# Performance work log

Hardware: AMD Instinct MI355X
Metric: run time of the kernel (lower is better)

The kernel has to match this reference:

```python
import jax, jax.numpy as jnp
import numpy as np

EMBED_DIM = 1024
N_HEADS = 16
HEAD_DIM = EMBED_DIM // N_HEADS


def setup_inputs() -> dict:
    key = jax.random.key(0)
    ks = jax.random.split(key, 8)
    B, Tq, Tk, C = 2, 2048, 2048, EMBED_DIM
    s = 1.0 / np.sqrt(C)
    return {
        "query": jax.random.normal(ks[0], (B, Tq, C), jnp.float32),
        "context": jax.random.normal(ks[1], (B, Tk, C), jnp.float32),
        "Wq": jax.random.normal(ks[2], (C, C), jnp.float32) * s,
        "bq": jnp.zeros((C,), jnp.float32),
        "Wkv": jax.random.normal(ks[3], (C, 2 * C), jnp.float32) * s,
        "bkv": jnp.zeros((2 * C,), jnp.float32),
        "Wo": jax.random.normal(ks[4], (C, C), jnp.float32) * s,
        "bo": jnp.zeros((C,), jnp.float32),
    }


def reference(query, context, Wq, bq, Wkv, bkv, Wo, bo):
    B, Tq, C = query.shape
    Tk = context.shape[1]
    H, D = N_HEADS, HEAD_DIM
    # projections
    q = (query @ Wq + bq).reshape(B, Tq, H, D)        # [B,Tq,H,D]
    kv = (context @ Wkv + bkv).reshape(B, Tk, 2, H, D)
    k = kv[:, :, 0]                                   # [B,Tk,H,D]
    v = kv[:, :, 1]
    scale = D ** -0.5
    # attention scores [B,H,Tq,Tk]
    attn = jnp.einsum("bqhd,bkhd->bhqk", q, k) * scale
    attn = jax.nn.softmax(attn, axis=-1)
    # dropout p=0.0 -> identity in eval / p=0
    out = jnp.einsum("bhqk,bkhd->bqhd", attn, v).reshape(B, Tq, C)
    return out @ Wo + bo
```

## Files before the change

kernel.cpp:

```cpp
#include <hip/hip_runtime.h>
#include <math.h>

typedef unsigned short u16;
typedef unsigned int u32;
typedef __attribute__((ext_vector_type(8))) short short8;
typedef __attribute__((ext_vector_type(4))) short short4v;
typedef __attribute__((ext_vector_type(4))) float f32x4;

__device__ __forceinline__ u16 f2bf(float f) {
  union { float f; unsigned u; } x; x.f = f;
  unsigned r = x.u + 0x7FFFu + ((x.u >> 16) & 1u);
  return (u16)(r >> 16);
}

__device__ __forceinline__ u32 asu(float f) {
  union { float f; u32 u; } x; x.f = f; return x.u;
}

__device__ __forceinline__ u32 pack2bf(float a, float b) {
  return __builtin_amdgcn_perm(asu(b) + 0x8000u, asu(a) + 0x8000u, 0x07060302u);
}

__device__ __forceinline__ void gld_lds16(const void* g, void* l) {
  __builtin_amdgcn_global_load_lds(
      (const __attribute__((address_space(1))) unsigned int*)g,
      (__attribute__((address_space(3))) unsigned int*)l, 16, 0, 0);
}

__global__ void pre_kernel(const float* __restrict__ q, const float* __restrict__ c,
                           const float* __restrict__ Wq, const float* __restrict__ Wkv,
                           const float* __restrict__ Wo,
                           u16* __restrict__ xq, u16* __restrict__ xc,
                           u16* __restrict__ WqT, u16* __restrict__ WkvT,
                           u16* __restrict__ WoT) {
  __shared__ float tile[32][33];
  int bx = blockIdx.x, t = threadIdx.x;
  if (bx < 8192) {
    int i = bx * 256 + t;
    const float* src = q; u16* dst = xq;
    if (i >= 1048576) { i -= 1048576; src = c; dst = xc; }
    float4 v = ((const float4*)src)[i];
    ((uint2*)dst)[i] = make_uint2(
        (unsigned)f2bf(v.x) | ((unsigned)f2bf(v.y) << 16),
        (unsigned)f2bf(v.z) | ((unsigned)f2bf(v.w) << 16));
  } else {
    int g = bx - 8192;
    int gx = g & 127, gy = g >> 7;
    const float* src; u16* dst; int N, n0;
    if (gx < 32)      { src = Wq;  dst = WqT;  N = 1024; n0 = gx * 32; }
    else if (gx < 96) { src = Wkv; dst = WkvT; N = 2048; n0 = (gx - 32) * 32; }
    else              { src = Wo;  dst = WoT;  N = 1024; n0 = (gx - 96) * 32; }
    int k0 = gy * 32;
    int tx = t & 31, ty = t >> 5;
#pragma unroll
    for (int i = 0; i < 4; ++i)
      tile[ty * 4 + i][tx] = src[(size_t)(k0 + ty * 4 + i) * N + n0 + tx];
    __syncthreads();
#pragma unroll
    for (int i = 0; i < 4; ++i)
      dst[(size_t)(n0 + ty * 4 + i) * 1024 + k0 + tx] = f2bf(tile[tx][ty * 4 + i]);
  }
}

__global__ __launch_bounds__(256) void qkv_gemm(
    const u16* __restrict__ Xq, const u16* __restrict__ Xc,
    const u16* __restrict__ WqT, const u16* __restrict__ WkvT,
    const float* __restrict__ bq, const float* __restrict__ bkv,
    u16* __restrict__ qb, u16* __restrict__ kf, u16* __restrict__ vf,
    float qscale) {
  __shared__ __align__(16) u16 smem[16896];
  u16* As = smem;
  u16* Bs = smem + 8192;
  const int tid = threadIdx.x, lane = tid & 63, wave = tid >> 6;
  const int quad = lane >> 4, cl = lane & 15;
  const int wr = (wave >> 1) * 64, wc = (wave & 1) * 64;

  int x = blockIdx.x;
  const u16 *A, *Bt; const float* bias; int N, m0, n0; bool isq;
  if (x < 256) {
    isq = true;  A = Xq; Bt = WqT;  bias = bq;  N = 1024;
    m0 = (x >> 3) * 128; n0 = (x & 7) * 128;
  } else {
    isq = false; x -= 256; A = Xc; Bt = WkvT; bias = bkv; N = 2048;
    m0 = (x >> 4) * 128; n0 = (x & 15) * 128;
  }

  f32x4 acc[4][4] = {};

  for (int k0 = 0; k0 < 1024; k0 += 64) {
#pragma unroll
    for (int it = 0; it < 4; ++it) {
      int chunk = (it * 4 + wave) * 64 + lane;
      int row = chunk >> 3, kc = (chunk & 7) * 8;
      gld_lds16(A + (size_t)(m0 + row) * 1024 + k0 + kc, As + (size_t)(it * 4 + wave) * 512);
      gld_lds16(Bt + (size_t)(n0 + row) * 1024 + k0 + kc, Bs + (size_t)(it * 4 + wave) * 512);
    }
    __syncthreads();
#pragma unroll
    for (int ks = 0; ks < 2; ++ks) {
      short8 af[4], bf[4];
#pragma unroll
      for (int mi = 0; mi < 4; ++mi)
        af[mi] = *(const short8*)(As + (wr + mi * 16 + cl) * 64 + ks * 32 + quad * 8);
#pragma unroll
      for (int ni = 0; ni < 4; ++ni)
        bf[ni] = *(const short8*)(Bs + (wc + ni * 16 + cl) * 64 + ks * 32 + quad * 8);
#pragma unroll
      for (int mi = 0; mi < 4; ++mi)
#pragma unroll
        for (int ni = 0; ni < 4; ++ni)
          acc[mi][ni] = __builtin_amdgcn_mfma_f32_16x16x32_bf16(af[mi], bf[ni], acc[mi][ni], 0, 0, 0);
    }
    __syncthreads();
  }

  if (isq) {
#pragma unroll
    for (int mi = 0; mi < 4; ++mi)
#pragma unroll
      for (int ni = 0; ni < 4; ++ni)
#pragma unroll
        for (int r = 0; r < 4; ++r) {
          int row = m0 + wr + mi * 16 + quad * 4 + r;
          int col = n0 + wc + ni * 16 + cl;
          qb[(size_t)row * 1024 + col] = f2bf((acc[mi][ni][r] + bias[col]) * qscale);
        }
    return;
  }

  const int b = m0 >> 11, kt0 = (m0 & 2047) >> 6;
  const bool kreg = (n0 < 1024);
  if (kreg) {
#pragma unroll
    for (int mi = 0; mi < 4; ++mi)
#pragma unroll
      for (int ni = 0; ni < 4; ++ni)
#pragma unroll
        for (int r = 0; r < 4; ++r)
          smem[(wr + mi * 16 + quad * 4 + r) * 132 + wc + ni * 16 + cl] =
              f2bf(acc[mi][ni][r] + bias[n0 + wc + ni * 16 + cl]);
    __syncthreads();
#pragma unroll
    for (int i = 0; i < 8; ++i) {
      int c = i * 4 + wave;
      int hs = c >> 4, ts = (c >> 3) & 1, ks = (c >> 2) & 1, idx = c & 3;
      int h = (n0 >> 6) + hs;
      size_t bhkt = ((size_t)((b * 16 + h) * 32 + kt0 + ts)) * 4096;
      short8 v = *(const short8*)(smem + (ts * 64 + idx * 16 + cl) * 132 +
                                  hs * 64 + ks * 32 + quad * 8);
      *(short8*)(kf + bhkt + (size_t)(ks * 4 + idx) * 512 + lane * 8) = v;
    }
  } else {
#pragma unroll
    for (int mi = 0; mi < 4; ++mi)
#pragma unroll
      for (int ni = 0; ni < 4; ++ni) {
        float v0 = acc[mi][ni][0] + bias[n0 + wc + ni * 16 + cl];
        float v1 = acc[mi][ni][1] + bias[n0 + wc + ni * 16 + cl];
        float v2 = acc[mi][ni][2] + bias[n0 + wc + ni * 16 + cl];
        float v3 = acc[mi][ni][3] + bias[n0 + wc + ni * 16 + cl];
        *(uint2*)(smem + (wc + ni * 16 + cl) * 132 + wr + mi * 16 + quad * 4) =
            make_uint2(pack2bf(v0, v1), pack2bf(v2, v3));
      }
    __syncthreads();
#pragma unroll
    for (int i = 0; i < 8; ++i) {
      int c = i * 4 + wave;
      int hs = c >> 4, ts = (c >> 3) & 1, ks = (c >> 2) & 1, idx = c & 3;
      int h = ((n0 - 1024) >> 6) + hs;
      size_t bhkt = ((size_t)((b * 16 + h) * 32 + kt0 + ts)) * 4096;
      const u16* src = smem + (hs * 64 + idx * 16 + cl) * 132 + ts * 64 + ks * 32 + quad * 4;
      short8 v;
      *(short4v*)&v       = *(const short4v*)(src);
      *((short4v*)&v + 1) = *(const short4v*)(src + 16);
      *(short8*)(vf + bhkt + (size_t)(ks * 4 + idx) * 512 + lane * 8) = v;
    }
  }
}

__global__ __launch_bounds__(512) void o_gemm(
    const u16* __restrict__ A, const u16* __restrict__ Bt,
    const float* __restrict__ bias, float* __restrict__ Cm) {
  __shared__ __align__(16) u16 As[128 * 64];
  __shared__ __align__(16) u16 Bs[128 * 64];
  const int tid = threadIdx.x, lane = tid & 63, wave = tid >> 6;
  const int quad = lane >> 4, cl = lane & 15;
  const int m0 = (blockIdx.x >> 3) * 128, n0 = (blockIdx.x & 7) * 128;
  const int wr = (wave >> 2) * 64, wc = (wave & 3) * 32;

  f32x4 acc[4][2] = {};

  for (int k0 = 0; k0 < 1024; k0 += 64) {
    const int rA = lane >> 3, kc = (lane & 7) * 8;
#pragma unroll
    for (int it = 0; it < 2; ++it) {
      int ch = it * 8 + wave;
      gld_lds16(A + (size_t)(m0 + ch * 8 + rA) * 1024 + k0 + kc, As + ch * 512);
    }
#pragma unroll
    for (int it = 0; it < 2; ++it) {
      int ch = it * 8 + wave;
      gld_lds16(Bt + (size_t)(n0 + ch * 8 + rA) * 1024 + k0 + kc, Bs + ch * 512);
    }
    __syncthreads();
#pragma unroll
    for (int ks = 0; ks < 2; ++ks) {
      short8 af[4], bf[2];
#pragma unroll
      for (int mi = 0; mi < 4; ++mi)
        af[mi] = *(const short8*)(As + (wr + mi * 16 + cl) * 64 + ks * 32 + quad * 8);
#pragma unroll
      for (int ni = 0; ni < 2; ++ni)
        bf[ni] = *(const short8*)(Bs + (wc + ni * 16 + cl) * 64 + ks * 32 + quad * 8);
#pragma unroll
      for (int mi = 0; mi < 4; ++mi)
#pragma unroll
        for (int ni = 0; ni < 2; ++ni)
          acc[mi][ni] = __builtin_amdgcn_mfma_f32_16x16x32_bf16(af[mi], bf[ni], acc[mi][ni], 0, 0, 0);
    }
    __syncthreads();
  }
#pragma unroll
  for (int mi = 0; mi < 4; ++mi)
#pragma unroll
    for (int ni = 0; ni < 2; ++ni)
#pragma unroll
      for (int r = 0; r < 4; ++r) {
        int row = m0 + wr + mi * 16 + quad * 4 + r;
        int col = n0 + wc + ni * 16 + cl;
        Cm[(size_t)row * 1024 + col] = acc[mi][ni][r] + bias[col];
      }
}

__global__ __launch_bounds__(256, 4) void flash_attn(
    const u16* __restrict__ qb, const u16* __restrict__ kf,
    const u16* __restrict__ vf, u16* __restrict__ outp) {
  __shared__ __align__(16) u16 kv[2][16 * 512];
  const int tid = threadIdx.x, lane = tid & 63, wave = tid >> 6;
  const int quad = lane >> 4, cl = lane & 15;
  const int id = blockIdx.x;
  const int h = (id & 7) | (((id >> 3) & 1) << 3);
  const int b = (id >> 4) & 1;
  const int qt = id >> 5;

  const int qrow0 = b * 2048 + qt * 64 + wave * 16;
  short8 bq[2];
#pragma unroll
  for (int ks = 0; ks < 2; ++ks)
    bq[ks] = *(const short8*)(qb + (size_t)(qrow0 + cl) * 1024 + h * 64 + ks * 32 + quad * 8);

  const u16* kfb = kf + (size_t)((b * 16 + h) * 32) * 4096;
  const u16* vfb = vf + (size_t)((b * 16 + h) * 32) * 4096;

  auto stage = [&](int kt, int buf) {
#pragma unroll
    for (int i = 0; i < 2; ++i) {
      int c = wave * 2 + i;
      gld_lds16(kfb + (size_t)kt * 4096 + c * 512 + lane * 8, &kv[buf][c * 512]);
      gld_lds16(vfb + (size_t)kt * 4096 + c * 512 + lane * 8, &kv[buf][(8 + c) * 512]);
    }
  };

  f32x4 o_acc[4] = {};
  float l_lane = 0.f;

  stage(0, 0);
  __syncthreads();

#pragma unroll 1
  for (int kt = 0; kt < 32; ++kt) {
    const int cur = kt & 1, nxt = cur ^ 1;
    if (kt < 31) stage(kt + 1, nxt);
    const u16* kb = &kv[cur][0];
    const u16* vb = &kv[cur][8 * 512];
    f32x4 st[4] = {};
#pragma unroll
    for (int ks = 0; ks < 2; ++ks)
#pragma unroll
      for (int ni = 0; ni < 4; ++ni) {
        short8 ak = *(const short8*)(kb + (ks * 4 + ni) * 512 + lane * 8);
        st[ni] = __builtin_amdgcn_mfma_f32_16x16x32_bf16(ak, bq[ks], st[ni], 0, 0, 0);
      }
    u32 bp[2][4];
#pragma unroll
    for (int ni = 0; ni < 4; ++ni) {
      float p0 = __builtin_amdgcn_exp2f(st[ni][0]);
      float p1 = __builtin_amdgcn_exp2f(st[ni][1]);
      float p2 = __builtin_amdgcn_exp2f(st[ni][2]);
      float p3 = __builtin_amdgcn_exp2f(st[ni][3]);
      l_lane += (p0 + p1) + (p2 + p3);
      bp[ni >> 1][(ni & 1) * 2 + 0] = pack2bf(p0, p1);
      bp[ni >> 1][(ni & 1) * 2 + 1] = pack2bf(p2, p3);
    }
#pragma unroll
    for (int ks = 0; ks < 2; ++ks) {
      short8 pb;
      *(u32*)&pb     = bp[ks][0];
      ((u32*)&pb)[1] = bp[ks][1];
      ((u32*)&pb)[2] = bp[ks][2];
      ((u32*)&pb)[3] = bp[ks][3];
#pragma unroll
      for (int nd = 0; nd < 4; ++nd) {
        short8 av = *(const short8*)(vb + (ks * 4 + nd) * 512 + lane * 8);
        o_acc[nd] = __builtin_amdgcn_mfma_f32_16x16x32_bf16(av, pb, o_acc[nd], 0, 0, 0);
      }
    }
    __syncthreads();
  }
  l_lane += __shfl_xor(l_lane, 16);
  l_lane += __shfl_xor(l_lane, 32);
  float inv = 1.f / l_lane;
  u16* Ow = &kv[0][wave * 16 * 68];
#pragma unroll
  for (int nd = 0; nd < 4; ++nd)
#pragma unroll
    for (int r2 = 0; r2 < 2; ++r2)
      *(u32*)(Ow + cl * 68 + nd * 16 + quad * 4 + r2 * 2) =
          pack2bf(o_acc[nd][r2 * 2] * inv, o_acc[nd][r2 * 2 + 1] * inv);
#pragma unroll
  for (int half = 0; half < 2; ++half) {
    int row = half * 8 + (lane >> 3);
    int d0 = (lane & 7) * 8;
    short8 ov = *(const short8*)(Ow + row * 68 + d0);
    *(short8*)(outp + (size_t)(qrow0 + row) * 1024 + h * 64 + d0) = ov;
  }
}

extern "C" void kernel_launch(void* const* d_in, const int* in_sizes, int n_in,
                              void* d_out, int out_size, void* d_ws, size_t ws_size,
                              hipStream_t stream) {
  const float* query   = (const float*)d_in[0];
  const float* context = (const float*)d_in[1];
  const float* Wq  = (const float*)d_in[2];
  const float* bq  = (const float*)d_in[3];
  const float* Wkv = (const float*)d_in[4];
  const float* bkv = (const float*)d_in[5];
  const float* Wo  = (const float*)d_in[6];
  const float* bo  = (const float*)d_in[7];
  float* out = (float*)d_out;

  char* ws = (char*)d_ws;
  size_t off = 0;
  auto alloc = [&](size_t bytes) {
    char* p = ws + off;
    off += (bytes + 255) & ~(size_t)255;
    return p;
  };
  u16* buf0 = (u16*)alloc(4096ull * 1024 * 2);
  u16* xcb  = (u16*)alloc(4096ull * 1024 * 2);
  u16* WqT  = (u16*)alloc(1024ull * 1024 * 2);
  u16* WkvT = (u16*)alloc(2048ull * 1024 * 2);
  u16* WoT  = (u16*)alloc(1024ull * 1024 * 2);
  u16* qb   = (u16*)alloc(4096ull * 1024 * 2);
  u16* kfr  = (u16*)alloc(4ull * 1024 * 1024 * 2);
  u16* vfr  = (u16*)alloc(4ull * 1024 * 1024 * 2);

  const float QSCALE = 0.125f * 1.44269504f;

  pre_kernel<<<12288, 256, 0, stream>>>(query, context, Wq, Wkv, Wo,
                                        buf0, xcb, WqT, WkvT, WoT);
  qkv_gemm<<<768, 256, 0, stream>>>(buf0, xcb, WqT, WkvT, bq, bkv,
                                    qb, kfr, vfr, QSCALE);
  flash_attn<<<1024, 256, 0, stream>>>(qb, kfr, vfr, buf0);
  o_gemm<<<256, 512, 0, stream>>>(buf0, WoT, bo, out);
}
```

Before: 225.4 us.

## Pre-swizzle weights into MFMA fragment layout and load B operands directly from global

The weight preprocessing now writes Wq, Wkv and Wo in bf16 as 16x32 MFMA-fragment tiles instead of a plain transpose. The QKV and output GEMMs then load B fragments straight from global memory into registers with coalesced 16-byte loads, skipping the LDS staging and LDS reads for B. This cuts LDS traffic and shared memory use, which could raise occupancy. The cost is that each wave loads weight fragments redundantly from global/L2 memory, and those loads are exposed before the barrier rather than overlapped.

```diff
diff --git a/kernel.cpp b/kernel.cpp
--- a/kernel.cpp
+++ b/kernel.cpp
@@ -31,10 +31,11 @@
                            const float* __restrict__ Wq, const float* __restrict__ Wkv,
                            const float* __restrict__ Wo,
                            u16* __restrict__ xq, u16* __restrict__ xc,
-                           u16* __restrict__ WqT, u16* __restrict__ WkvT,
-                           u16* __restrict__ WoT) {
+                           u16* __restrict__ WqF, u16* __restrict__ WkvF,
+                           u16* __restrict__ WoF) {
   __shared__ float tile[32][33];
-  int bx = blockIdx.x, t = threadIdx.x;
+  int bx = blockIdx.x;
+  int t = threadIdx.y * 32 + threadIdx.x;
   if (bx < 8192) {
     int i = bx * 256 + t;
     const float* src = q; u16* dst = xq;
@@ -47,69 +48,78 @@
     int g = bx - 8192;
     int gx = g & 127, gy = g >> 7;
     const float* src; u16* dst; int N, n0;
-    if (gx < 32)      { src = Wq;  dst = WqT;  N = 1024; n0 = gx * 32; }
-    else if (gx < 96) { src = Wkv; dst = WkvT; N = 2048; n0 = (gx - 32) * 32; }
-    else              { src = Wo;  dst = WoT;  N = 1024; n0 = (gx - 96) * 32; }
+    if (gx < 32)      { src = Wq;  dst = WqF;  N = 1024; n0 = gx * 32; }
+    else if (gx < 96) { src = Wkv; dst = WkvF; N = 2048; n0 = (gx - 32) * 32; }
+    else              { src = Wo;  dst = WoF;  N = 1024; n0 = (gx - 96) * 32; }
     int k0 = gy * 32;
-    int tx = t & 31, ty = t >> 5;
+    int tx = threadIdx.x, ty = threadIdx.y;
 #pragma unroll
     for (int i = 0; i < 4; ++i)
       tile[ty * 4 + i][tx] = src[(size_t)(k0 + ty * 4 + i) * N + n0 + tx];
     __syncthreads();
-#pragma unroll
-    for (int i = 0; i < 4; ++i)
-      dst[(size_t)(n0 + ty * 4 + i) * 1024 + k0 + tx] = f2bf(tile[tx][ty * 4 + i]);
+    int e = t * 4;
+    int ch = e >> 9, rem = e & 511;
+    int kg = (rem >> 7) & 3;
+    int nl = (rem >> 3) & 15;
+    int j0 = rem & 7;
+    int kk = kg * 8 + j0;
+    int nn = ch * 16 + nl;
+    u32 lo = pack2bf(tile[kk][nn], tile[kk + 1][nn]);
+    u32 hi = pack2bf(tile[kk + 2][nn], tile[kk + 3][nn]);
+    *(uint2*)(dst + (size_t)(((n0 >> 4) + ch) * 32 + gy) * 512 + rem) = make_uint2(lo, hi);
   }
 }
 
 __global__ __launch_bounds__(256) void qkv_gemm(
     const u16* __restrict__ Xq, const u16* __restrict__ Xc,
-    const u16* __restrict__ WqT, const u16* __restrict__ WkvT,
+    const u16* __restrict__ WqF, const u16* __restrict__ WkvF,
     const float* __restrict__ bq, const float* __restrict__ bkv,
     u16* __restrict__ qb, u16* __restrict__ kf, u16* __restrict__ vf,
     float qscale) {
   __shared__ __align__(16) u16 smem[16896];
   u16* As = smem;
-  u16* Bs = smem + 8192;
   const int tid = threadIdx.x, lane = tid & 63, wave = tid >> 6;
   const int quad = lane >> 4, cl = lane & 15;
   const int wr = (wave >> 1) * 64, wc = (wave & 1) * 64;
 
   int x = blockIdx.x;
-  const u16 *A, *Bt; const float* bias; int N, m0, n0; bool isq;
+  const u16 *A, *Bf; const float* bias; int m0, n0; bool isq;
   if (x < 256) {
-    isq = true;  A = Xq; Bt = WqT;  bias = bq;  N = 1024;
+    isq = true;  A = Xq; Bf = WqF;  bias = bq;
     m0 = (x >> 3) * 128; n0 = (x & 7) * 128;
   } else {
-    isq = false; x -= 256; A = Xc; Bt = WkvT; bias = bkv; N = 2048;
+    isq = false; x -= 256; A = Xc; Bf = WkvF; bias = bkv;
     m0 = (x >> 4) * 128; n0 = (x & 15) * 128;
   }
+  const int bn4 = (n0 + wc) >> 4;
 
   f32x4 acc[4][4] = {};
 
   for (int k0 = 0; k0 < 1024; k0 += 64) {
+    const int rA = lane >> 3, kc = (lane & 7) * 8;
 #pragma unroll
     for (int it = 0; it < 4; ++it) {
-      int chunk = (it * 4 + wave) * 64 + lane;
-      int row = chunk >> 3, kc = (chunk & 7) * 8;
-      gld_lds16(A + (size_t)(m0 + row) * 1024 + k0 + kc, As + (size_t)(it * 4 + wave) * 512);
-      gld_lds16(Bt + (size_t)(n0 + row) * 1024 + k0 + kc, Bs + (size_t)(it * 4 + wave) * 512);
-    }
+      int chunk = it * 4 + wave;
+      gld_lds16(A + (size_t)(m0 + chunk * 8 + rA) * 1024 + k0 + kc, As + chunk * 512);
+    }
+    short8 bf[2][4];
+#pragma unroll
+    for (int ks = 0; ks < 2; ++ks)
+#pragma unroll
+      for (int ni = 0; ni < 4; ++ni)
+        bf[ks][ni] = *(const short8*)(Bf + (size_t)((bn4 + ni) * 32 + (k0 >> 5) + ks) * 512 + lane * 8);
     __syncthreads();
 #pragma unroll
     for (int ks = 0; ks < 2; ++ks) {
-      short8 af[4], bf[4];
+      short8 af[4];
 #pragma unroll
       for (int mi = 0; mi < 4; ++mi)
         af[mi] = *(const short8*)(As + (wr + mi * 16 + cl) * 64 + ks * 32 + quad * 8);
 #pragma unroll
-      for (int ni = 0; ni < 4; ++ni)
-        bf[ni] = *(const short8*)(Bs + (wc + ni * 16 + cl) * 64 + ks * 32 + quad * 8);
-#pragma unroll
       for (int mi = 0; mi < 4; ++mi)
 #pragma unroll
         for (int ni = 0; ni < 4; ++ni)
-          acc[mi][ni] = __builtin_amdgcn_mfma_f32_16x16x32_bf16(af[mi], bf[ni], acc[mi][ni], 0, 0, 0);
+          acc[mi][ni] = __builtin_amdgcn_mfma_f32_16x16x32_bf16(af[mi], bf[ks][ni], acc[mi][ni], 0, 0, 0);
     }
     __syncthreads();
   }
@@ -179,14 +189,14 @@
 }
 
 __global__ __launch_bounds__(512) void o_gemm(
-    const u16* __restrict__ A, const u16* __restrict__ Bt,
+    const u16* __restrict__ A, const u16* __restrict__ Bf,
     const float* __restrict__ bias, float* __restrict__ Cm) {
   __shared__ __align__(16) u16 As[128 * 64];
-  __shared__ __align__(16) u16 Bs[128 * 64];
   const int tid = threadIdx.x, lane = tid & 63, wave = tid >> 6;
   const int quad = lane >> 4, cl = lane & 15;
   const int m0 = (blockIdx.x >> 3) * 128, n0 = (blockIdx.x & 7) * 128;
   const int wr = (wave >> 2) * 64, wc = (wave & 3) * 32;
+  const int bn4 = (n0 + wc) >> 4;
 
   f32x4 acc[4][2] = {};
 
@@ -197,26 +207,24 @@
       int ch = it * 8 + wave;
       gld_lds16(A + (size_t)(m0 + ch * 8 + rA) * 1024 + k0 + kc, As + ch * 512);
     }
-#pragma unroll
-    for (int it = 0; it < 2; ++it) {
-      int ch = it * 8 + wave;
-      gld_lds16(Bt + (size_t)(n0 + ch * 8 + rA) * 1024 + k0 + kc, Bs + ch * 512);
-    }
+    short8 bf[2][2];
+#pragma unroll
+    for (int ks = 0; ks < 2; ++ks)
+#pragma unroll
+      for (int ni = 0; ni < 2; ++ni)
+        bf[ks][ni] = *(const short8*)(Bf + (size_t)((bn4 + ni) * 32 + (k0 >> 5) + ks) * 512 + lane * 8);
     __syncthreads();
 #pragma unroll
     for (int ks = 0; ks < 2; ++ks) {
-      short8 af[4], bf[2];
+      short8 af[4];
 #pragma unroll
       for (int mi = 0; mi < 4; ++mi)
         af[mi] = *(const short8*)(As + (wr + mi * 16 + cl) * 64 + ks * 32 + quad * 8);
 #pragma unroll
-      for (int ni = 0; ni < 2; ++ni)
-        bf[ni] = *(const short8*)(Bs + (wc + ni * 16 + cl) * 64 + ks * 32 + quad * 8);
-#pragma unroll
       for (int mi = 0; mi < 4; ++mi)
 #pragma unroll
         for (int ni = 0; ni < 2; ++ni)
-          acc[mi][ni] = __builtin_amdgcn_mfma_f32_16x16x32_bf16(af[mi], bf[ni], acc[mi][ni], 0, 0, 0);
+          acc[mi][ni] = __builtin_amdgcn_mfma_f32_16x16x32_bf16(af[mi], bf[ks][ni], acc[mi][ni], 0, 0, 0);
     }
     __syncthreads();
   }
@@ -348,19 +356,19 @@
   };
   u16* buf0 = (u16*)alloc(4096ull * 1024 * 2);
   u16* xcb  = (u16*)alloc(4096ull * 1024 * 2);
-  u16* WqT  = (u16*)alloc(1024ull * 1024 * 2);
-  u16* WkvT = (u16*)alloc(2048ull * 1024 * 2);
-  u16* WoT  = (u16*)alloc(1024ull * 1024 * 2);
+  u16* WqF  = (u16*)alloc(1024ull * 1024 * 2);
+  u16* WkvF = (u16*)alloc(2048ull * 1024 * 2);
+  u16* WoF  = (u16*)alloc(1024ull * 1024 * 2);
   u16* qb   = (u16*)alloc(4096ull * 1024 * 2);
   u16* kfr  = (u16*)alloc(4ull * 1024 * 1024 * 2);
   u16* vfr  = (u16*)alloc(4ull * 1024 * 1024 * 2);
 
   const float QSCALE = 0.125f * 1.44269504f;
 
-  pre_kernel<<<12288, 256, 0, stream>>>(query, context, Wq, Wkv, Wo,
-                                        buf0, xcb, WqT, WkvT, WoT);
-  qkv_gemm<<<768, 256, 0, stream>>>(buf0, xcb, WqT, WkvT, bq, bkv,
+  pre_kernel<<<12288, dim3(32, 8), 0, stream>>>(query, context, Wq, Wkv, Wo,
+                                                buf0, xcb, WqF, WkvF, WoF);
+  qkv_gemm<<<768, 256, 0, stream>>>(buf0, xcb, WqF, WkvF, bq, bkv,
                                     qb, kfr, vfr, QSCALE);
   flash_attn<<<1024, 256, 0, stream>>>(qb, kfr, vfr, buf0);
-  o_gemm<<<256, 512, 0, stream>>>(buf0, WoT, bo, out);
-}
+  o_gemm<<<256, 512, 0, stream>>>(buf0, WoF, bo, out);
+}
```

Result: faster. 213.5 us (-5.2%).
